# Kernel tuning notes

Hardware: AMD Instinct MI355X
Metric: run time of the kernel (lower is better)

## Reference

```python
import jax, jax.numpy as jnp
import numpy as np

D = 128
N = 8192

def setup_inputs() -> dict:
    key = jax.random.key(0)
    k1, k2, k3 = jax.random.split(key, 3)
    return {
        "query": jax.random.normal(k1, (D, N), dtype=jnp.float32),
        "key": jax.random.normal(k2, (D, N), dtype=jnp.float32),
        "value": jax.random.normal(k3, (D, N), dtype=jnp.float32),
    }

def reference(query, key, value):
    # query, key, value: [d, N] (feature-major, as in the torch module)
    # scores[q, k] = sum_d query[d, q] * key[d, k]  -- NOTE: unscaled (no 1/sqrt(d))
    scores = jnp.einsum("dq,dk->qk", query, key)          # [Nq, Nk]
    p_attn = jax.nn.softmax(scores, axis=-1)               # [Nq, Nk]
    p_val = jnp.einsum("qk,dk->dq", p_attn, value)        # [d, Nq]
    return p_val
```

## Files before the change

kernel.cpp:

```cpp
#include <hip/hip_runtime.h>

#define NN 8192
#define DD 128
#define KSPLIT 16
#define KCHUNK (NN / KSPLIT)
#define BK 32
#define NT (KCHUNK / BK)
#define NTILES (NN / BK)
#define TILE_B 16384
#define OFF_V 8192
#define WAVES 4
#define BQ (WAVES * 32)

#define WS_M   ((size_t)NTILES * TILE_B)
#define WS_L   (WS_M + (size_t)KSPLIT * NN * 4)
#define WS_OP  (WS_L + (size_t)KSPLIT * NN * 4)
#define WS_NEED (WS_OP + (size_t)KSPLIT * NN * DD * 2)

typedef __attribute__((ext_vector_type(8))) _Float16 f16x8;
typedef __attribute__((ext_vector_type(2))) _Float16 f16x2;
typedef __attribute__((ext_vector_type(8))) short bf16x8;
typedef __attribute__((ext_vector_type(4))) float f32x4;
typedef __attribute__((ext_vector_type(2))) float f32x2;
typedef __attribute__((ext_vector_type(16))) float f32x16;

static __device__ __forceinline__ unsigned short f2bf(float f) {
    union { float f; unsigned u; } v; v.f = f;
    return (unsigned short)((v.u + 0x7FFFu + ((v.u >> 16) & 1u)) >> 16);
}
static __device__ __forceinline__ float bf2f(unsigned short h) {
    union { unsigned u; float f; } v; v.u = ((unsigned)h) << 16;
    return v.f;
}
static __device__ __forceinline__ void gld_lds16(const char* g, char* l) {
    __builtin_amdgcn_global_load_lds(
        (const __attribute__((address_space(1))) unsigned*)g,
        (__attribute__((address_space(3))) unsigned*)l,
        16, 0, 0);
}

__global__ __launch_bounds__(256) void attn_prep(
    const float* __restrict__ Km, const float* __restrict__ Vm,
    char* __restrict__ kst)
{
    __shared__ __align__(16) char img[TILE_B];
    const int tt = blockIdx.x;
    const int tid = threadIdx.x;
    const int k0 = tt * BK;
    #pragma unroll
    for (int i = 0; i < 16; ++i) {
        int idx = i * 256 + tid;
        int d = idx >> 5, k = idx & 31;
        float kv = Km[(size_t)d * NN + k0 + k];
        int b = (k * 256 + d * 2) ^ ((k & 7) << 4);
        *(_Float16*)(img + b) = (_Float16)kv;
    }
    #pragma unroll
    for (int i = 0; i < 16; ++i) {
        int idx = i * 256 + tid;
        int d = idx >> 5, j = idx & 31;
        int kl = (j & 3) + 4 * ((j >> 3) & 1) + 8 * ((j >> 2) & 1) + 16 * (j >> 4);
        float vv = Vm[(size_t)d * NN + k0 + kl];
        int b = (d * 64 + j * 2) ^ ((d & 7) << 4);
        *(_Float16*)(img + OFF_V + b) = (_Float16)vv;
    }
    __syncthreads();
    float4* dst = (float4*)(kst + (size_t)tt * TILE_B);
    const float4* src = (const float4*)img;
    #pragma unroll
    for (int i = 0; i < 4; ++i) dst[i * 256 + tid] = src[i * 256 + tid];
}

__global__ __launch_bounds__(256, 3) void attn_main(
    const float* __restrict__ Qm, const char* __restrict__ kst,
    float* __restrict__ mArr, float* __restrict__ lArr,
    _Float16* __restrict__ opart)
{
    __shared__ __align__(16) char smem[2 * TILE_B];
    const int tid = threadIdx.x;
    const int wave = tid >> 6, lane = tid & 63;
    const int q31 = lane & 31;
    const int h = lane >> 5;
    const int swz = (lane & 7) << 4;
    const int ks = blockIdx.x & (KSPLIT - 1);
    const int qb = blockIdx.x >> 4;
    const int q0w = qb * BQ + wave * 32;
    const int qg = q0w + q31;
    const float LOG2E = 1.44269504088896340736f;

    f16x8 qh[8];
    #pragma unroll
    for (int ds = 0; ds < 8; ++ds)
        #pragma unroll
        for (int jj = 0; jj < 8; ++jj) {
            int d = 16 * ds + 8 * h + jj;
            qh[ds][jj] = (_Float16)(Qm[(size_t)d * NN + qg] * LOG2E);
        }

    f32x16 acc[4];
    #pragma unroll
    for (int dt = 0; dt < 4; ++dt)
        #pragma unroll
        for (int r = 0; r < 16; ++r) acc[dt][r] = 0.f;
    float mrun = -INFINITY, lrun = 0.f;

    {
        const char* gsrc = kst + (size_t)(ks * NT) * TILE_B + tid * 16;
        char* ldst = smem + tid * 16;
        #pragma unroll
        for (int i = 0; i < 4; ++i) gld_lds16(gsrc + i * 4096, ldst + i * 4096);
    }
    __syncthreads();

    for (int t = 0; t < NT; ++t) {
        const int cur = t & 1;
        const char* kb = smem + cur * TILE_B;

        if (t + 1 < NT) {
            const char* gsrc = kst + (size_t)(ks * NT + t + 1) * TILE_B + tid * 16;
            char* ldst = smem + (cur ^ 1) * TILE_B + tid * 16;
            #pragma unroll
            for (int i = 0; i < 4; ++i) gld_lds16(gsrc + i * 4096, ldst + i * 4096);
        }

        f32x16 T;
        #pragma unroll
        for (int r = 0; r < 16; ++r) T[r] = 0.f;
        __builtin_amdgcn_s_setprio(1);
        #pragma unroll
        for (int ds = 0; ds < 8; ++ds) {
            int off = ((q31 << 8) + ds * 32 + (h << 4)) ^ swz;
            f16x8 kh = *(const f16x8*)(kb + off);
            T = __builtin_amdgcn_mfma_f32_32x32x16_f16(kh, qh[ds], T, 0, 0, 0);
        }
        __builtin_amdgcn_s_setprio(0);

        float tmax = fmaxf(T[0], T[1]);
        #pragma unroll
        for (int r = 2; r < 16; ++r) tmax = fmaxf(tmax, T[r]);
        tmax = fmaxf(tmax, __shfl_xor(tmax, 32, 64));

        if (__any(tmax > mrun)) {
            float mnew = fmaxf(mrun, tmax);
            float sc = __builtin_amdgcn_exp2f(mrun - mnew);
            mrun = mnew;
            lrun *= sc;
            #pragma unroll
            for (int dt = 0; dt < 4; ++dt)
                #pragma unroll
                for (int r = 0; r < 16; ++r) acc[dt][r] *= sc;
        }

        f16x8 pfrag[2];
        float psum = 0.f;
        #pragma unroll
        for (int s2 = 0; s2 < 2; ++s2)
            #pragma unroll
            for (int jj = 0; jj < 8; ++jj) {
                float p = __builtin_amdgcn_exp2f(T[8 * s2 + jj] - mrun);
                psum += p;
                pfrag[s2][jj] = (_Float16)p;
            }
        lrun += psum;

        __builtin_amdgcn_s_setprio(1);
        #pragma unroll
        for (int dt = 0; dt < 4; ++dt) {
            int vbase = (dt * 32 + q31) * 64 + (h << 4);
            #pragma unroll
            for (int s2 = 0; s2 < 2; ++s2) {
                f16x8 vb = *(const f16x8*)(kb + OFF_V + ((vbase + s2 * 32) ^ swz));
                acc[dt] = __builtin_amdgcn_mfma_f32_32x32x16_f16(vb, pfrag[s2], acc[dt], 0, 0, 0);
            }
        }
        __builtin_amdgcn_s_setprio(0);

        __syncthreads();
    }

    lrun += __shfl_xor(lrun, 32, 64);
    if (lane < 32) {
        mArr[ks * NN + qg] = mrun;
        lArr[ks * NN + qg] = lrun;
    }
    #pragma unroll
    for (int dt = 0; dt < 4; ++dt)
        #pragma unroll
        for (int r = 0; r < 16; ++r) {
            int d = dt * 32 + (r & 3) + 8 * (r >> 2) + 4 * h;
            opart[((size_t)ks * DD + d) * NN + qg] = (_Float16)acc[dt][r];
        }
}

__global__ __launch_bounds__(256) void attn_combine(
    const _Float16* __restrict__ opart, const float* __restrict__ mArr,
    const float* __restrict__ lArr, float* __restrict__ out)
{
    const int tid = threadIdx.x;
    const int qg = blockIdx.x >> 3;
    const int dseg = (blockIdx.x & 7) * 16;
    const int q = qg * 512 + tid * 2;

    f32x2 mv[KSPLIT];
    float M0 = -INFINITY, M1 = -INFINITY;
    #pragma unroll
    for (int s = 0; s < KSPLIT; ++s) {
        mv[s] = *(const f32x2*)&mArr[(size_t)s * NN + q];
        M0 = fmaxf(M0, mv[s][0]);
        M1 = fmaxf(M1, mv[s][1]);
    }
    float L0 = 0.f, L1 = 0.f;
    f32x2 w[KSPLIT];
    #pragma unroll
    for (int s = 0; s < KSPLIT; ++s) {
        f32x2 lv = *(const f32x2*)&lArr[(size_t)s * NN + q];
        w[s][0] = __builtin_amdgcn_exp2f(mv[s][0] - M0);
        w[s][1] = __builtin_amdgcn_exp2f(mv[s][1] - M1);
        L0 += w[s][0] * lv[0];
        L1 += w[s][1] * lv[1];
    }
    float i0 = 1.f / L0, i1 = 1.f / L1;
    #pragma unroll
    for (int s = 0; s < KSPLIT; ++s) { w[s][0] *= i0; w[s][1] *= i1; }

    for (int dd = 0; dd < 16; ++dd) {
        int d = dseg + dd;
        float a0 = 0.f, a1 = 0.f;
        #pragma unroll
        for (int s = 0; s < KSPLIT; ++s) {
            f16x2 u = *(const f16x2*)&opart[((size_t)s * DD + d) * NN + q];
            a0 += w[s][0] * (float)u[0];
            a1 += w[s][1] * (float)u[1];
        }
        f32x2 o; o[0] = a0; o[1] = a1;
        *(f32x2*)&out[(size_t)d * NN + q] = o;
    }
}

__global__ __launch_bounds__(512, 2) void attn_fwd_fb(
    const float* __restrict__ Qm, const float* __restrict__ Km,
    const float* __restrict__ Vm, float* __restrict__ out)
{
    const int tid  = threadIdx.x;
    const int wave = tid >> 6;
    const int lane = tid & 63;
    const int c = lane & 15;
    const int g = lane >> 4;
    const int q0 = blockIdx.x * 32;
    const float LOG2E = 1.44269504088896340736f;

    bf16x8 qhi[2][4], qlo[2][4];
    #pragma unroll
    for (int qt = 0; qt < 2; ++qt)
        #pragma unroll
        for (int ds = 0; ds < 4; ++ds)
            #pragma unroll
            for (int jj = 0; jj < 8; ++jj) {
                int d = ds * 32 + 8 * g + jj;
                float qv = Qm[(size_t)d * NN + (q0 + qt * 16 + c)] * LOG2E;
                unsigned short hv = f2bf(qv);
                qhi[qt][ds][jj] = (short)hv;
                qlo[qt][ds][jj] = (short)f2bf(qv - bf2f(hv));
            }

    f32x4 acc[2][8];
    #pragma unroll
    for (int a = 0; a < 2; ++a)
        #pragma unroll
        for (int b = 0; b < 8; ++b)
            acc[a][b] = (f32x4){0.f, 0.f, 0.f, 0.f};
    float mrun[2] = {-INFINITY, -INFINITY};
    float lrun[2] = {0.f, 0.f};
    const int kw0 = wave * (NN / 8);

    for (int t = 0; t < (NN / 8) / 64; ++t) {
        const int k0 = kw0 + t * 64;
        f32x4 T[4][2];
        #pragma unroll
        for (int mkt = 0; mkt < 4; ++mkt) {
            T[mkt][0] = (f32x4){0.f, 0.f, 0.f, 0.f};
            T[mkt][1] = (f32x4){0.f, 0.f, 0.f, 0.f};
        }
        #pragma unroll
        for (int mkt = 0; mkt < 4; ++mkt) {
            const int kc = k0 + mkt * 16 + c;
            #pragma unroll
            for (int ds = 0; ds < 4; ++ds) {
                bf16x8 khi, klo;
                #pragma unroll
                for (int jj = 0; jj < 8; ++jj) {
                    int d = ds * 32 + 8 * g + jj;
                    float kv = Km[(size_t)d * NN + kc];
                    unsigned short hv = f2bf(kv);
                    khi[jj] = (short)hv;
                    klo[jj] = (short)f2bf(kv - bf2f(hv));
                }
                #pragma unroll
                for (int qt = 0; qt < 2; ++qt) {
                    T[mkt][qt] = __builtin_amdgcn_mfma_f32_16x16x32_bf16(khi, qhi[qt][ds], T[mkt][qt], 0, 0, 0);
                    T[mkt][qt] = __builtin_amdgcn_mfma_f32_16x16x32_bf16(khi, qlo[qt][ds], T[mkt][qt], 0, 0, 0);
                    T[mkt][qt] = __builtin_amdgcn_mfma_f32_16x16x32_bf16(klo, qhi[qt][ds], T[mkt][qt], 0, 0, 0);
                }
            }
        }
        bf16x8 pfrag[2][2];
        float scl[2];
        #pragma unroll
        for (int qt = 0; qt < 2; ++qt) {
            float tmax = T[0][qt][0];
            #pragma unroll
            for (int mkt = 0; mkt < 4; ++mkt)
                #pragma unroll
                for (int r = 0; r < 4; ++r)
                    tmax = fmaxf(tmax, T[mkt][qt][r]);
            tmax = fmaxf(tmax, __shfl_xor(tmax, 16, 64));
            tmax = fmaxf(tmax, __shfl_xor(tmax, 32, 64));
            float mnew = fmaxf(mrun[qt], tmax);
            float sc = __builtin_amdgcn_exp2f(mrun[qt] - mnew);
            mrun[qt] = mnew;
            lrun[qt] *= sc;
            scl[qt] = sc;
            #pragma unroll
            for (int s = 0; s < 2; ++s)
                #pragma unroll
                for (int hf = 0; hf < 2; ++hf) {
                    int mkt = 2 * s + hf;
                    #pragma unroll
                    for (int r = 0; r < 4; ++r) {
                        float p = __builtin_amdgcn_exp2f(T[mkt][qt][r] - mnew);
                        unsigned short pb = f2bf(p);
                        lrun[qt] += bf2f(pb);
                        pfrag[qt][s][hf * 4 + r] = (short)pb;
                    }
                }
        }
        #pragma unroll
        for (int qt = 0; qt < 2; ++qt)
            #pragma unroll
            for (int r = 0; r < 4; ++r) {
                float f = __shfl(scl[qt], 4 * g + r, 64);
                #pragma unroll
                for (int dt = 0; dt < 8; ++dt)
                    acc[qt][dt][r] *= f;
            }
        #pragma unroll
        for (int s = 0; s < 2; ++s)
            #pragma unroll
            for (int dt = 0; dt < 8; ++dt) {
                const float* vp = Vm + (size_t)(dt * 16 + c) * NN + (k0 + 32 * s + 4 * g);
                f32x4 v0 = *(const f32x4*)vp;
                f32x4 v1 = *(const f32x4*)(vp + 16);
                bf16x8 vb;
                #pragma unroll
                for (int e = 0; e < 4; ++e) {
                    vb[e]     = (short)f2bf(v0[e]);
                    vb[4 + e] = (short)f2bf(v1[e]);
                }
                #pragma unroll
                for (int qt = 0; qt < 2; ++qt)
                    acc[qt][dt] = __builtin_amdgcn_mfma_f32_16x16x32_bf16(pfrag[qt][s], vb, acc[qt][dt], 0, 0, 0);
            }
    }

    __shared__ float obuf[32][DD + 4];
    __shared__ float mbuf[8][32];
    __shared__ float lbuf[8][32];
    __shared__ float lsbuf[32];
    #pragma unroll
    for (int qt = 0; qt < 2; ++qt) {
        lrun[qt] += __shfl_xor(lrun[qt], 16, 64);
        lrun[qt] += __shfl_xor(lrun[qt], 32, 64);
    }
    if (lane < 16) {
        mbuf[wave][c]      = mrun[0];
        mbuf[wave][16 + c] = mrun[1];
        lbuf[wave][c]      = lrun[0];
        lbuf[wave][16 + c] = lrun[1];
    }
    for (int i = tid; i < 32 * (DD + 4); i += 512)
        (&obuf[0][0])[i] = 0.f;
    __syncthreads();
    float fac[2];
    {
        float lst[2];
        #pragma unroll
        for (int qt = 0; qt < 2; ++qt) {
            int q = qt * 16 + c;
            float mm = -INFINITY;
            #pragma unroll
            for (int w = 0; w < 8; ++w) mm = fmaxf(mm, mbuf[w][q]);
            float ls = 0.f;
            #pragma unroll
            for (int w = 0; w < 8; ++w)
                ls += __builtin_amdgcn_exp2f(mbuf[w][q] - mm) * lbuf[w][q];
            fac[qt] = __builtin_amdgcn_exp2f(mrun[qt] - mm);
            lst[qt] = ls;
        }
        if (wave == 0 && lane < 16) {
            lsbuf[c]      = lst[0];
            lsbuf[16 + c] = lst[1];
        }
    }
    float facr[2][4];
    #pragma unroll
    for (int qt = 0; qt < 2; ++qt)
        #pragma unroll
        for (int r = 0; r < 4; ++r)
            facr[qt][r] = __shfl(fac[qt], 4 * g + r, 64);
    for (int w = 0; w < 8; ++w) {
        if (wave == w) {
            #pragma unroll
            for (int qt = 0; qt < 2; ++qt)
                #pragma unroll
                for (int dt = 0; dt < 8; ++dt)
                    #pragma unroll
                    for (int r = 0; r < 4; ++r)
                        obuf[qt * 16 + 4 * g + r][dt * 16 + c] += facr[qt][r] * acc[qt][dt][r];
        }
        __syncthreads();
    }
    const int qq = tid & 31;
    const int dg = tid >> 5;
    const float inv = 1.f / lsbuf[qq];
    #pragma unroll
    for (int i = 0; i < 8; ++i) {
        int d = dg * 8 + i;
        out[(size_t)d * NN + q0 + qq] = obuf[qq][d] * inv;
    }
}

extern "C" void kernel_launch(void* const* d_in, const int* in_sizes, int n_in,
                              void* d_out, int out_size, void* d_ws, size_t ws_size,
                              hipStream_t stream) {
    const float* Q = (const float*)d_in[0];
    const float* K = (const float*)d_in[1];
    const float* V = (const float*)d_in[2];
    float* out = (float*)d_out;

    if (ws_size < WS_NEED || d_ws == nullptr) {
        hipLaunchKernelGGL(attn_fwd_fb, dim3(NN / 32), dim3(512), 0, stream, Q, K, V, out);
        return;
    }
    char* ws = (char*)d_ws;
    char* kst = ws;
    float* mArr = (float*)(ws + WS_M);
    float* lArr = (float*)(ws + WS_L);
    _Float16* opart = (_Float16*)(ws + WS_OP);

    hipLaunchKernelGGL(attn_prep, dim3(NTILES), dim3(256), 0, stream, K, V, kst);
    hipLaunchKernelGGL(attn_main, dim3(KSPLIT * (NN / BQ)), dim3(256), 0, stream, Q, kst, mArr, lArr, opart);
    hipLaunchKernelGGL(attn_combine, dim3((NN / 512) * 8), dim3(256), 0, stream, opart, mArr, lArr, out);
}
```

Measured before the change: 71.15 us.

## Widen LDS swizzle, raise occupancy, split QK accumulators, packed fp16 convert

The LDS XOR swizzle widens from 8 to 16 rows in both the prep and main kernels, to cut bank conflicts on the K and V tile reads. The launch bounds go from 3 to 4 blocks per CU, which raises occupancy but squeezes the per-thread register budget. The QK^T MFMA chain is split into two independent accumulators that are summed afterwards, to break the serial dependency between MFMAs. Max and sum reductions become tree-shaped, and P is packed with cvt_pkrtz, which rounds toward zero instead of to nearest.

```diff
diff --git a/kernel.cpp b/kernel.cpp
--- a/kernel.cpp
+++ b/kernel.cpp
@@ -19,6 +19,7 @@
 
 typedef __attribute__((ext_vector_type(8))) _Float16 f16x8;
 typedef __attribute__((ext_vector_type(2))) _Float16 f16x2;
+typedef __attribute__((ext_vector_type(2))) __fp16 fp16v2;
 typedef __attribute__((ext_vector_type(8))) short bf16x8;
 typedef __attribute__((ext_vector_type(4))) float f32x4;
 typedef __attribute__((ext_vector_type(2))) float f32x2;
@@ -52,7 +53,7 @@
         int idx = i * 256 + tid;
         int d = idx >> 5, k = idx & 31;
         float kv = Km[(size_t)d * NN + k0 + k];
-        int b = (k * 256 + d * 2) ^ ((k & 7) << 4);
+        int b = (k * 256 + d * 2) ^ ((k & 15) << 4);
         *(_Float16*)(img + b) = (_Float16)kv;
     }
     #pragma unroll
@@ -61,7 +62,7 @@
         int d = idx >> 5, j = idx & 31;
         int kl = (j & 3) + 4 * ((j >> 3) & 1) + 8 * ((j >> 2) & 1) + 16 * (j >> 4);
         float vv = Vm[(size_t)d * NN + k0 + kl];
-        int b = (d * 64 + j * 2) ^ ((d & 7) << 4);
+        int b = (d * 64 + j * 2) ^ ((d & 15) << 4);
         *(_Float16*)(img + OFF_V + b) = (_Float16)vv;
     }
     __syncthreads();
@@ -71,7 +72,7 @@
     for (int i = 0; i < 4; ++i) dst[i * 256 + tid] = src[i * 256 + tid];
 }
 
-__global__ __launch_bounds__(256, 3) void attn_main(
+__global__ __launch_bounds__(256, 4) void attn_main(
     const float* __restrict__ Qm, const char* __restrict__ kst,
     float* __restrict__ mArr, float* __restrict__ lArr,
     _Float16* __restrict__ opart)
@@ -81,7 +82,7 @@
     const int wave = tid >> 6, lane = tid & 63;
     const int q31 = lane & 31;
     const int h = lane >> 5;
-    const int swz = (lane & 7) << 4;
+    const int swz = (q31 & 15) << 4;
     const int ks = blockIdx.x & (KSPLIT - 1);
     const int qb = blockIdx.x >> 4;
     const int q0w = qb * BQ + wave * 32;
@@ -104,11 +105,13 @@
         for (int r = 0; r < 16; ++r) acc[dt][r] = 0.f;
     float mrun = -INFINITY, lrun = 0.f;
 
+    const char* kwg = kst + (size_t)(ks * NT) * TILE_B + tid * 16;
+
     {
-        const char* gsrc = kst + (size_t)(ks * NT) * TILE_B + tid * 16;
-        char* ldst = smem + tid * 16;
-        #pragma unroll
-        for (int i = 0; i < 4; ++i) gld_lds16(gsrc + i * 4096, ldst + i * 4096);
+        const char* gs = kwg;
+        char* ld = smem + tid * 16;
+        #pragma unroll
+        for (int i = 0; i < 4; ++i) gld_lds16(gs + i * 4096, ld + i * 4096);
     }
     __syncthreads();
 
@@ -117,61 +120,71 @@
         const char* kb = smem + cur * TILE_B;
 
         if (t + 1 < NT) {
-            const char* gsrc = kst + (size_t)(ks * NT + t + 1) * TILE_B + tid * 16;
-            char* ldst = smem + (cur ^ 1) * TILE_B + tid * 16;
-            #pragma unroll
-            for (int i = 0; i < 4; ++i) gld_lds16(gsrc + i * 4096, ldst + i * 4096);
-        }
-
+            const char* gs = kwg + (size_t)(t + 1) * TILE_B;
+            char* ld = smem + (cur ^ 1) * TILE_B + tid * 16;
+            #pragma unroll
+            for (int i = 0; i < 4; ++i) gld_lds16(gs + i * 4096, ld + i * 4096);
+        }
+
+        f32x16 Ta, Tb;
+        #pragma unroll
+        for (int r = 0; r < 16; ++r) { Ta[r] = 0.f; Tb[r] = 0.f; }
+        __builtin_amdgcn_s_setprio(1);
+        #pragma unroll
+        for (int ds = 0; ds < 4; ++ds) {
+            int offA = ((q31 << 8) + (2 * ds) * 32 + (h << 4)) ^ swz;
+            int offB = ((q31 << 8) + (2 * ds + 1) * 32 + (h << 4)) ^ swz;
+            f16x8 ka = *(const f16x8*)(kb + offA);
+            f16x8 kb2 = *(const f16x8*)(kb + offB);
+            Ta = __builtin_amdgcn_mfma_f32_32x32x16_f16(ka, qh[2 * ds], Ta, 0, 0, 0);
+            Tb = __builtin_amdgcn_mfma_f32_32x32x16_f16(kb2, qh[2 * ds + 1], Tb, 0, 0, 0);
+        }
+        __builtin_amdgcn_s_setprio(0);
         f32x16 T;
         #pragma unroll
-        for (int r = 0; r < 16; ++r) T[r] = 0.f;
-        __builtin_amdgcn_s_setprio(1);
-        #pragma unroll
-        for (int ds = 0; ds < 8; ++ds) {
-            int off = ((q31 << 8) + ds * 32 + (h << 4)) ^ swz;
-            f16x8 kh = *(const f16x8*)(kb + off);
-            T = __builtin_amdgcn_mfma_f32_32x32x16_f16(kh, qh[ds], T, 0, 0, 0);
-        }
-        __builtin_amdgcn_s_setprio(0);
-
-        float tmax = fmaxf(T[0], T[1]);
-        #pragma unroll
-        for (int r = 2; r < 16; ++r) tmax = fmaxf(tmax, T[r]);
+        for (int r = 0; r < 16; ++r) T[r] = Ta[r] + Tb[r];
+
+        float a0 = fmaxf(fmaxf(T[0], T[1]), T[2]);
+        float a1 = fmaxf(fmaxf(T[3], T[4]), T[5]);
+        float a2 = fmaxf(fmaxf(T[6], T[7]), T[8]);
+        float a3 = fmaxf(fmaxf(T[9], T[10]), T[11]);
+        float a4 = fmaxf(fmaxf(T[12], T[13]), T[14]);
+        float tmax = fmaxf(fmaxf(fmaxf(a0, a1), a2), fmaxf(fmaxf(a3, a4), T[15]));
         tmax = fmaxf(tmax, __shfl_xor(tmax, 32, 64));
 
         if (__any(tmax > mrun)) {
             float mnew = fmaxf(mrun, tmax);
             float sc = __builtin_amdgcn_exp2f(mrun - mnew);
-            mrun = mnew;
-            lrun *= sc;
+            mrun = mnew; lrun *= sc;
             #pragma unroll
             for (int dt = 0; dt < 4; ++dt)
                 #pragma unroll
                 for (int r = 0; r < 16; ++r) acc[dt][r] *= sc;
         }
 
-        f16x8 pfrag[2];
-        float psum = 0.f;
-        #pragma unroll
-        for (int s2 = 0; s2 < 2; ++s2)
-            #pragma unroll
-            for (int jj = 0; jj < 8; ++jj) {
-                float p = __builtin_amdgcn_exp2f(T[8 * s2 + jj] - mrun);
-                psum += p;
-                pfrag[s2][jj] = (_Float16)p;
-            }
-        lrun += psum;
-
+        float p[16];
+        #pragma unroll
+        for (int r = 0; r < 16; ++r)
+            p[r] = __builtin_amdgcn_exp2f(T[r] - mrun);
+        float s0 = (p[0] + p[1]) + (p[2] + p[3]);
+        float s1 = (p[4] + p[5]) + (p[6] + p[7]);
+        float s2 = (p[8] + p[9]) + (p[10] + p[11]);
+        float s3 = (p[12] + p[13]) + (p[14] + p[15]);
+        lrun += (s0 + s1) + (s2 + s3);
+        union { f16x8 v[2]; fp16v2 h2[8]; } pu;
+        #pragma unroll
+        for (int r = 0; r < 8; ++r)
+            pu.h2[r] = __builtin_amdgcn_cvt_pkrtz(p[2 * r], p[2 * r + 1]);
+
+        const char* vb = kb + OFF_V;
         __builtin_amdgcn_s_setprio(1);
         #pragma unroll
         for (int dt = 0; dt < 4; ++dt) {
             int vbase = (dt * 32 + q31) * 64 + (h << 4);
-            #pragma unroll
-            for (int s2 = 0; s2 < 2; ++s2) {
-                f16x8 vb = *(const f16x8*)(kb + OFF_V + ((vbase + s2 * 32) ^ swz));
-                acc[dt] = __builtin_amdgcn_mfma_f32_32x32x16_f16(vb, pfrag[s2], acc[dt], 0, 0, 0);
-            }
+            f16x8 v0 = *(const f16x8*)(vb + ((vbase) ^ swz));
+            f16x8 v1 = *(const f16x8*)(vb + ((vbase + 32) ^ swz));
+            acc[dt] = __builtin_amdgcn_mfma_f32_32x32x16_f16(v0, pu.v[0], acc[dt], 0, 0, 0);
+            acc[dt] = __builtin_amdgcn_mfma_f32_32x32x16_f16(v1, pu.v[1], acc[dt], 0, 0, 0);
         }
         __builtin_amdgcn_s_setprio(0);
 
@@ -327,8 +340,8 @@
                     int mkt = 2 * s + hf;
                     #pragma unroll
                     for (int r = 0; r < 4; ++r) {
-                        float p = __builtin_amdgcn_exp2f(T[mkt][qt][r] - mnew);
-                        unsigned short pb = f2bf(p);
+                        float pv = __builtin_amdgcn_exp2f(T[mkt][qt][r] - mnew);
+                        unsigned short pb = f2bf(pv);
                         lrun[qt] += bf2f(pb);
                         pfrag[qt][s][hf * 4 + r] = (short)pb;
                     }
@@ -350,15 +363,15 @@
                 const float* vp = Vm + (size_t)(dt * 16 + c) * NN + (k0 + 32 * s + 4 * g);
                 f32x4 v0 = *(const f32x4*)vp;
                 f32x4 v1 = *(const f32x4*)(vp + 16);
-                bf16x8 vb;
+                bf16x8 vbf;
                 #pragma unroll
                 for (int e = 0; e < 4; ++e) {
-                    vb[e]     = (short)f2bf(v0[e]);
-                    vb[4 + e] = (short)f2bf(v1[e]);
+                    vbf[e]     = (short)f2bf(v0[e]);
+                    vbf[4 + e] = (short)f2bf(v1[e]);
                 }
                 #pragma unroll
                 for (int qt = 0; qt < 2; ++qt)
-                    acc[qt][dt] = __builtin_amdgcn_mfma_f32_16x16x32_bf16(pfrag[qt][s], vb, acc[qt][dt], 0, 0, 0);
+                    acc[qt][dt] = __builtin_amdgcn_mfma_f32_16x16x32_bf16(pfrag[qt][s], vbf, acc[qt][dt], 0, 0, 0);
             }
     }
 
```

New measurement: 121.7 us (median of 4 runs). +71.0%, slower.
